# Optimization experiments

Hardware: AMD Instinct MI355X
Metric: run time of the kernel (lower is better)

## Reference

```python
import jax, jax.numpy as jnp
import numpy as np

IN_CH = 256
NUM_CLASSES = 1
CONF_THR = 0.3
NMS_IOU = 0.2
ANCHOR_SIZES = (32.0, 64.0, 128.0)
ASPECTS = (0.5, 1.0, 2.0)
NUM_ANCHORS = len(ANCHOR_SIZES) * len(ASPECTS)  # 9
K_CAND = 1024   # top-score candidates fed to NMS per image
MAX_DET = 100   # max_output_size in source
BN_EPS = 1e-5


def _anchors():
    a = [[s * r / 224.0, s / r / 224.0] for s in ANCHOR_SIZES for r in ASPECTS]
    return jnp.asarray(a, jnp.float32)  # [A, 2] (w, h)


def _conv(x, w, b, pad):
    y = jax.lax.conv_general_dilated(x, w, (1, 1), [(pad, pad), (pad, pad)],
                                     dimension_numbers=('NCHW', 'OIHW', 'NCHW'))
    return y + b[None, :, None, None]


def _bn(x, g, b, m, v):
    inv = jax.lax.rsqrt(v + BN_EPS)
    return (x - m[None, :, None, None]) * (g * inv)[None, :, None, None] + b[None, :, None, None]


def _corners(b):
    return (b[..., 0] - b[..., 2] / 2, b[..., 1] - b[..., 3] / 2,
            b[..., 0] + b[..., 2] / 2, b[..., 1] + b[..., 3] / 2)


def _iou_one(box, boxes):
    # box: [4] cxcywh, boxes: [K,4] -> iou [K]
    ax1, ay1, ax2, ay2 = _corners(box)
    bx1, by1, bx2, by2 = _corners(boxes)
    iw = jnp.maximum(jnp.minimum(ax2, bx2) - jnp.maximum(ax1, bx1), 0.0)
    ih = jnp.maximum(jnp.minimum(ay2, by2) - jnp.maximum(ay1, by1), 0.0)
    inter = iw * ih
    union = (ax2 - ax1) * (ay2 - ay1) + (bx2 - bx1) * (by2 - by1) - inter
    return inter / (union + 1e-16)


def _nms(boxes, scores):
    # boxes [K,4], scores [K] -> kept boxes padded to [MAX_DET,4]
    s0 = jnp.where(scores > CONF_THR, scores, -1.0)

    def body(i, carry):
        s, out = carry
        j = jnp.argmax(s)
        ok = s[j] > 0.0
        box = boxes[j]
        iou = _iou_one(box, boxes)
        s_new = jnp.where(iou > NMS_IOU, -1.0, s).at[j].set(-1.0)
        s = jnp.where(ok, s_new, s)
        out = out.at[i].set(jnp.where(ok, box, jnp.zeros_like(box)))
        return s, out

    _, out = jax.lax.fori_loop(0, MAX_DET, body,
                               (s0, jnp.zeros((MAX_DET, 4), boxes.dtype)))
    return out


def _forward(features, w1, b1, g1, be1, m1, v1, w2, b2, g2, be2, m2, v2, wo, bo):
    x = jax.nn.relu(_bn(_conv(features, w1, b1, 1), g1, be1, m1, v1))
    x = jax.nn.relu(_bn(_conv(x, w2, b2, 1), g2, be2, m2, v2))
    p = _conv(x, wo, bo, 0)                      # [B, A*(5+C), H, W]
    B, _, H, W = p.shape
    p = p.reshape(B, NUM_ANCHORS, 5 + NUM_CLASSES, H, W).transpose(0, 3, 4, 1, 2)  # [B,H,W,A,5+C]
    obj = jax.nn.sigmoid(p[..., 4])
    anch = _anchors()
    gx = jnp.arange(W, dtype=p.dtype)[None, :, None]
    gy = jnp.arange(H, dtype=p.dtype)[:, None, None]
    px = (jax.nn.sigmoid(p[..., 0]) + gx) / W
    py = (jax.nn.sigmoid(p[..., 1]) + gy) / H
    pw = jnp.exp(p[..., 2]) * anch[:, 0]
    ph = jnp.exp(p[..., 3]) * anch[:, 1]
    boxes = jnp.stack([px, py, pw, ph], -1).reshape(B, -1, 4)
    if NUM_CLASSES > 1:
        scores = obj * jax.nn.sigmoid(p[..., 5:]).max(-1)
    else:
        scores = obj
    scores = scores.reshape(B, -1)

    def per_image(bx, sc):
        top_s, idx = jax.lax.top_k(sc, K_CAND)
        return _nms(bx[idx], top_s)

    return jax.vmap(per_image)(boxes, scores)    # [B, MAX_DET, 4]


def setup_inputs() -> dict:
    key = jax.random.key(0)
    ks = jax.random.split(key, 16)
    B = 32
    c1, c2 = IN_CH // 2, IN_CH // 4
    oc = NUM_ANCHORS * (5 + NUM_CLASSES)
    return {
        'features': jax.random.normal(ks[0], (B, IN_CH, 56, 56), jnp.float32),
        'w1': jax.random.normal(ks[1], (c1, IN_CH, 3, 3), jnp.float32) * 0.02,
        'b1': jax.random.normal(ks[2], (c1,), jnp.float32) * 0.02,
        'g1': 1.0 + 0.1 * jax.random.normal(ks[3], (c1,), jnp.float32),
        'be1': 0.1 * jax.random.normal(ks[4], (c1,), jnp.float32),
        'm1': 0.1 * jax.random.normal(ks[5], (c1,), jnp.float32),
        'v1': jax.random.uniform(ks[6], (c1,), jnp.float32, 0.5, 1.5),
        'w2': jax.random.normal(ks[7], (c2, c1, 3, 3), jnp.float32) * 0.03,
        'b2': jax.random.normal(ks[8], (c2,), jnp.float32) * 0.02,
        'g2': 1.0 + 0.1 * jax.random.normal(ks[9], (c2,), jnp.float32),
        'be2': 0.1 * jax.random.normal(ks[10], (c2,), jnp.float32),
        'm2': 0.1 * jax.random.normal(ks[11], (c2,), jnp.float32),
        'v2': jax.random.uniform(ks[12], (c2,), jnp.float32, 0.5, 1.5),
        'wo': jax.random.normal(ks[13], (oc, c2, 1, 1), jnp.float32) * 0.1,
        'bo': jax.random.normal(ks[14], (oc,), jnp.float32) * 0.05,
    }


def reference(features, w1, b1, g1, be1, m1, v1, w2, b2, g2, be2, m2, v2, wo, bo):
    return _forward(features, w1, b1, g1, be1, m1, v1, w2, b2, g2, be2, m2, v2, wo, bo)
```

## Files before the change

### kernel.cpp

```cpp
#include <hip/hip_runtime.h>
#include <math.h>

constexpr int BB   = 32;
constexpr int HW   = 3136;
constexpr int C0   = 256, C1 = 128, C2 = 64;
constexpr int NA   = 9;
constexpr int NCAND = HW * NA;
constexpr int KSEL  = 1024;
constexpr int MAXDET = 100;

typedef _Float16 half8 __attribute__((ext_vector_type(8)));
typedef _Float16 half4v __attribute__((ext_vector_type(4)));
typedef float    f32x4  __attribute__((ext_vector_type(4)));
typedef float    f32x16 __attribute__((ext_vector_type(16)));

__global__ void bn_prep(const float* __restrict__ g, const float* __restrict__ be,
                        const float* __restrict__ m, const float* __restrict__ v,
                        const float* __restrict__ cb,
                        float* __restrict__ scl, float* __restrict__ tb, int n) {
    int i = threadIdx.x;
    if (i < n) {
        float inv = 1.f / sqrtf(v[i] + 1e-5f);
        float s = g[i] * inv;
        scl[i] = s;
        tb[i] = be[i] + (cb[i] - m[i]) * s;
    }
}

__global__ void reorder_w6(const float* __restrict__ w, _Float16* __restrict__ wc,
                           int CIN, int COUT) {
    int i = blockIdx.x * 256 + threadIdx.x;
    int K = CIN * 9;
    if (i >= 2 * COUT * K) return;
    int ci  = i & 31;
    int row = (i >> 5) % (2 * COUT);
    int ch  = (i >> 5) / (2 * COUT);
    int pl  = row / COUT;
    int oc  = row - pl * COUT;
    int cg = ch / 9, r = ch - cg * 9;
    int cin = cg * 32 + ci;
    float v = w[oc * K + cin * 9 + r];
    _Float16 h = (_Float16)v;
    wc[i] = pl ? (_Float16)(v - (float)h) : h;
}

__global__ __launch_bounds__(256) void nchw_to_nhwc_split(
    const float* __restrict__ in, _Float16* __restrict__ hi, _Float16* __restrict__ lo)
{
    __shared__ float tile[64 * 68];
    const int pt = blockIdx.x * 64, ct = blockIdx.y * 64, b = blockIdx.z;
    const int t = threadIdx.x;
    const int r0 = t >> 4, cidx = (t & 15) * 4;
#pragma unroll
    for (int rr = 0; rr < 64; rr += 16) {
        int r = rr + r0;
        const float* src = in + ((size_t)(b * 256 + ct + r)) * HW + pt + cidx;
        float4 v = *(const float4*)src;
        float* d = &tile[r * 68 + cidx];
        d[0] = v.x; d[1] = v.y; d[2] = v.z; d[3] = v.w;
    }
    __syncthreads();
    const int p = t >> 2, c0 = (t & 3) * 16;
    size_t obase = ((size_t)(b * HW + pt + p)) * 256 + ct + c0;
    half8 h0, h1, l0, l1;
#pragma unroll
    for (int j = 0; j < 16; ++j) {
        float v = tile[(c0 + j) * 68 + p];
        _Float16 hh = (_Float16)v;
        _Float16 ll = (_Float16)(v - (float)hh);
        if (j < 8) { h0[j] = hh; l0[j] = ll; }
        else       { h1[j - 8] = hh; l1[j - 8] = ll; }
    }
    *(half8*)(hi + obase)     = h0;
    *(half8*)(hi + obase + 8) = h1;
    *(half8*)(lo + obase)     = l0;
    *(half8*)(lo + obase + 8) = l1;
}

template <int CIN, int COUT, bool NHWC_OUT>
__global__ __launch_bounds__(256, 3) void conv3x3_v7(
    const _Float16* __restrict__ xhi,
    const _Float16* __restrict__ xlo,
    const _Float16* __restrict__ wc,
    const float* __restrict__ scl, const float* __restrict__ tb,
    _Float16* __restrict__ ohi,
    _Float16* __restrict__ olo,
    float* __restrict__ onchw)
{
    constexpr int K     = CIN * 9;
    constexpr int NCH   = K / 32;
    constexpr int WROWS = 2 * COUT;
    constexpr int WOC   = (COUT / 64) ? (COUT / 64) : 1;
    constexpr int PROW  = 72;
    constexpr int WROW  = 40;
    constexpr int WLDS  = WROWS / 64;

    __shared__ _Float16 SP[128 * PROW];
    __shared__ _Float16 SW[WROWS * WROW];

    const int bid = blockIdx.x;
    const int swz = (bid & 7) * (gridDim.x >> 3) + (bid >> 3);
    const int b = swz / 25;
    const int pixBase = (swz - b * 25) * 128;
    const int bHW = b * HW;

    const int t = threadIdx.x;

    const int p     = t & 127;
    const int plane = t >> 7;
    const int pixA  = pixBase + p;
    const int ya = pixA / 56, xa = pixA - ya * 56;
    const bool pv = pixA < HW;
    const _Float16* xsrc = plane ? xlo : xhi;

    const int l = t & 63;
    const int wid = t >> 6;
    const int wp = wid & 1, wo = wid >> 1;
    const int lc = l & 31, lk = l >> 5;

    f32x16 acc[2][WOC];
#pragma unroll
    for (int pi = 0; pi < 2; ++pi)
#pragma unroll
        for (int oi = 0; oi < WOC; ++oi) acc[pi][oi] = (f32x16)0.f;

    half8 pld[4];
    half8 wld[WLDS];

    auto stage_issue = [&](int ch) {
        int cg = ch / 9, r = ch - cg * 9;
        int ky = r / 3, kx = r - ky * 3;
        int iy = ya + ky - 1, ix = xa + kx - 1;
        bool valid = pv && ((unsigned)iy < 56u) && ((unsigned)ix < 56u);
        int sp = pixA + (ky - 1) * 56 + (kx - 1);
        const _Float16* src = xsrc + (valid ? ((size_t)(bHW + sp)) * CIN + cg * 32 : 0);
#pragma unroll
        for (int q = 0; q < 4; ++q) pld[q] = *(const half8*)(src + q * 8);
        if (!valid) {
#pragma unroll
            for (int q = 0; q < 4; ++q)
#pragma unroll
                for (int j = 0; j < 8; ++j) pld[q][j] = (_Float16)0.f;
        }
        const _Float16* wsA = wc + (size_t)ch * WROWS * 32 + t * (WLDS * 8);
#pragma unroll
        for (int q = 0; q < WLDS; ++q) wld[q] = *(const half8*)(wsA + q * 8);
    };
    auto stage_write = [&]() {
#pragma unroll
        for (int q = 0; q < 4; ++q)
            *(half8*)&SP[p * PROW + plane * 32 + q * 8] = pld[q];
#pragma unroll
        for (int q = 0; q < WLDS; ++q) {
            int h0 = t * (WLDS * 8) + q * 8;
            *(half8*)&SW[(h0 >> 5) * WROW + (h0 & 31)] = wld[q];
        }
    };

    stage_issue(0);
    stage_write();
    __syncthreads();

    for (int ch = 0; ch < NCH; ++ch) {
        const bool more = (ch + 1) < NCH;
        if (more) stage_issue(ch + 1);

#pragma unroll
        for (int ks = 0; ks < 2; ++ks) {
            half8 pb[2][2];
#pragma unroll
            for (int pi = 0; pi < 2; ++pi) {
                int prw = wp * 64 + pi * 32 + lc;
#pragma unroll
                for (int pl2 = 0; pl2 < 2; ++pl2)
                    pb[pi][pl2] = *(const half8*)&SP[prw * PROW + pl2 * 32 + ks * 16 + lk * 8];
            }
            half8 wa[WOC][2];
#pragma unroll
            for (int oi = 0; oi < WOC; ++oi) {
#pragma unroll
                for (int pl2 = 0; pl2 < 2; ++pl2) {
                    int row = pl2 * COUT + wo * (WOC * 32) + oi * 32 + lc;
                    wa[oi][pl2] = *(const half8*)&SW[row * WROW + ks * 16 + lk * 8];
                }
            }
#pragma unroll
            for (int pi = 0; pi < 2; ++pi)
#pragma unroll
                for (int oi = 0; oi < WOC; ++oi) {
                    acc[pi][oi] = __builtin_amdgcn_mfma_f32_32x32x16_f16(wa[oi][0], pb[pi][0], acc[pi][oi], 0, 0, 0);
                    acc[pi][oi] = __builtin_amdgcn_mfma_f32_32x32x16_f16(wa[oi][0], pb[pi][1], acc[pi][oi], 0, 0, 0);
                    acc[pi][oi] = __builtin_amdgcn_mfma_f32_32x32x16_f16(wa[oi][1], pb[pi][0], acc[pi][oi], 0, 0, 0);
                }
        }
        __syncthreads();
        if (more) {
            stage_write();
            __syncthreads();
        }
    }

#pragma unroll
    for (int pi = 0; pi < 2; ++pi) {
        const int pix = pixBase + wp * 64 + pi * 32 + lc;
        if (pix < HW) {
#pragma unroll
            for (int oi = 0; oi < WOC; ++oi) {
#pragma unroll
                for (int g = 0; g < 4; ++g) {
                    const int oc0 = wo * (WOC * 32) + oi * 32 + 8 * g + 4 * lk;
                    f32x4 s4 = *(const f32x4*)(scl + oc0);
                    f32x4 t4 = *(const f32x4*)(tb + oc0);
                    if constexpr (NHWC_OUT) {
                        half4v hh, ll;
#pragma unroll
                        for (int m2 = 0; m2 < 4; ++m2) {
                            float val = fmaxf(acc[pi][oi][g * 4 + m2] * s4[m2] + t4[m2], 0.f);
                            _Float16 h = (_Float16)val;
                            hh[m2] = h;
                            ll[m2] = (_Float16)(val - (float)h);
                        }
                        size_t o = ((size_t)(bHW + pix)) * COUT + oc0;
                        *(half4v*)(ohi + o) = hh;
                        *(half4v*)(olo + o) = ll;
                    } else {
#pragma unroll
                        for (int m2 = 0; m2 < 4; ++m2) {
                            float val = fmaxf(acc[pi][oi][g * 4 + m2] * s4[m2] + t4[m2], 0.f);
                            onchw[((size_t)(b * COUT + oc0 + m2)) * HW + pix] = val;
                        }
                    }
                }
            }
        }
    }
}

__global__ __launch_bounds__(256) void conv1x1_decode(
    const float* __restrict__ x2, const float* __restrict__ wo,
    const float* __restrict__ bo,
    float* __restrict__ boxes, float* __restrict__ scores)
{
    __shared__ float ws[64 * 56];
    for (int i = threadIdx.x; i < 54 * 64; i += 256) {
        int oc = i % 54, c = i / 54;
        ws[c * 56 + oc] = wo[oc * 64 + c];
    }
    __syncthreads();

    int u = blockIdx.x * 256 + threadIdx.x;
    int a = u % 9;
    int rest = u / 9;
    int quad = rest % 784;
    int b = rest / 784;
    int pix0 = quad * 4;
    int y = pix0 / 56;
    int x0 = pix0 - y * 56;

    const float* xb = x2 + (size_t)b * 64 * HW + pix0;
    float acc[5][4];
#pragma unroll
    for (int j = 0; j < 5; ++j)
#pragma unroll
        for (int p = 0; p < 4; ++p) acc[j][p] = 0.f;

#pragma unroll 8
    for (int c = 0; c < 64; ++c) {
        float4 xv = *(const float4*)(xb + c * HW);
#pragma unroll
        for (int j = 0; j < 5; ++j) {
            float w = ws[c * 56 + a * 6 + j];
            acc[j][0] += w * xv.x;
            acc[j][1] += w * xv.y;
            acc[j][2] += w * xv.z;
            acc[j][3] += w * xv.w;
        }
    }

    int si = a / 3, ri = a - si * 3;
    float sv = (float)(32 << si);
    float rv = 0.5f * (float)(1 << ri);
    float aw = (sv * rv) / 224.f;
    float ah = (sv / rv) / 224.f;
    float bo0 = bo[a * 6 + 0], bo1 = bo[a * 6 + 1], bo2 = bo[a * 6 + 2];
    float bo3 = bo[a * 6 + 3], bo4 = bo[a * 6 + 4];

#pragma unroll
    for (int p = 0; p < 4; ++p) {
        float p0 = acc[0][p] + bo0;
        float p1 = acc[1][p] + bo1;
        float p2 = acc[2][p] + bo2;
        float p3 = acc[3][p] + bo3;
        float p4 = acc[4][p] + bo4;
        float sx = 1.f / (1.f + expf(-p0));
        float sy = 1.f / (1.f + expf(-p1));
        float pxc = (sx + (float)(x0 + p)) / 56.f;
        float pyc = (sy + (float)y) / 56.f;
        float pw = expf(p2) * aw;
        float ph = expf(p3) * ah;
        float sc = 1.f / (1.f + expf(-p4));
        int n = (y * 56 + x0 + p) * 9 + a;
        float4 bx; bx.x = pxc; bx.y = pyc; bx.z = pw; bx.w = ph;
        *(float4*)&boxes[((size_t)b * NCAND + n) * 4] = bx;
        scores[(size_t)b * NCAND + n] = sc;
    }
}

__device__ __forceinline__ unsigned fkey(float f) {
    unsigned u = __float_as_uint(f);
    return (u & 0x80000000u) ? ~u : (u | 0x80000000u);
}

__global__ __launch_bounds__(1024) void topk_select(
    const float* __restrict__ scores, const float* __restrict__ boxes,
    float* __restrict__ cbox, float* __restrict__ csc, int* __restrict__ cidx)
{
    const int b = blockIdx.x, t = threadIdx.x;
    const float* sp = scores + (size_t)b * NCAND;
    const int lane = t & 63, w = t >> 6;

    __shared__ unsigned hist[256];
    __shared__ unsigned wsum[16];
    __shared__ unsigned s_sel, s_need, s_tot0, s_tot1;

    unsigned prefix = 0, maskSo = 0;
    int need = KSEL;

    for (int round = 0; round < 4; ++round) {
        int shift = 24 - round * 8;
        if (t < 256) hist[t] = 0;
        __syncthreads();
        for (int i = t; i < NCAND; i += 1024) {
            unsigned u = fkey(sp[i]);
            if ((u & maskSo) == prefix) atomicAdd(&hist[(u >> shift) & 255], 1u);
        }
        __syncthreads();
        if (t == 0) {
            int rem = need;
            unsigned sel = 0;
            for (int v = 255; v >= 0; --v) {
                int c = (int)hist[v];
                if (c >= rem) { sel = (unsigned)v; break; }
                rem -= c;
            }
            s_sel = sel; s_need = (unsigned)rem;
        }
        __syncthreads();
        prefix |= (s_sel << shift);
        maskSo |= (0xFFu << shift);
        need = (int)s_need;
        __syncthreads();
    }

    const unsigned cutoff = prefix;
    const unsigned needT = (unsigned)need;
    unsigned outBase = 0, tieBase = 0;
    const unsigned long long mlt = (1ull << lane) - 1ull;

    for (int c0 = 0; c0 < NCAND; c0 += 1024) {
        int i = c0 + t;
        bool valid = i < NCAND;
        float sc = valid ? sp[i] : 0.f;
        unsigned u = valid ? fkey(sc) : 0u;
        bool gt = valid && (u > cutoff);
        bool eq = valid && (u == cutoff);

        unsigned long long balE = __ballot(eq);
        unsigned lpE = (unsigned)__popcll(balE & mlt);
        if (lane == 0) wsum[w] = (unsigned)__popcll(balE);
        __syncthreads();
        if (t == 0) {
            unsigned run = 0;
            for (int k = 0; k < 16; ++k) { unsigned x = wsum[k]; wsum[k] = run; run += x; }
            s_tot1 = run;
        }
        __syncthreads();
        unsigned tieRank = tieBase + wsum[w] + lpE;
        bool take = gt || (eq && tieRank < needT);
        __syncthreads();

        unsigned long long balT = __ballot(take);
        unsigned lpT = (unsigned)__popcll(balT & mlt);
        if (lane == 0) wsum[w] = (unsigned)__popcll(balT);
        __syncthreads();
        if (t == 0) {
            unsigned run = 0;
            for (int k = 0; k < 16; ++k) { unsigned x = wsum[k]; wsum[k] = run; run += x; }
            s_tot0 = run;
        }
        __syncthreads();
        unsigned pos = outBase + wsum[w] + lpT;
        if (take) {
            float4 bx = *(const float4*)&boxes[((size_t)b * NCAND + i) * 4];
            *(float4*)&cbox[((size_t)b * KSEL + pos) * 4] = bx;
            csc[(size_t)b * KSEL + pos] = sc;
            cidx[(size_t)b * KSEL + pos] = i;
        }
        tieBase += s_tot1;
        outBase += s_tot0;
        __syncthreads();
    }
}

__global__ __launch_bounds__(64) void nms_wave(
    const float* __restrict__ cbox, const float* __restrict__ csc,
    const int* __restrict__ cidx, float* __restrict__ out)
{
    const int b = blockIdx.x, l = threadIdx.x;
    float cx[16], cy[16], w_[16], h_[16], s[16];
    int id[16];
#pragma unroll
    for (int j = 0; j < 16; ++j) {
        int ci = (b << 10) + (j << 6) + l;
        float4 bb = *(const float4*)&cbox[(size_t)ci * 4];
        float sc = csc[ci];
        cx[j] = bb.x; cy[j] = bb.y; w_[j] = bb.z; h_[j] = bb.w;
        s[j] = sc > 0.3f ? sc : -1.f;
        id[j] = cidx[ci];
    }
    float* ob = out + (size_t)b * MAXDET * 4;

    for (int it = 0; it < MAXDET; ++it) {
        float bs = s[0]; int bi = id[0];
        float bcx = cx[0], bcy = cy[0], bw = w_[0], bh = h_[0];
#pragma unroll
        for (int j = 1; j < 16; ++j) {
            bool tk = (s[j] > bs) || (s[j] == bs && id[j] < bi);
            if (tk) { bs = s[j]; bi = id[j]; bcx = cx[j]; bcy = cy[j]; bw = w_[j]; bh = h_[j]; }
        }
#pragma unroll
        for (int m2 = 1; m2 < 64; m2 <<= 1) {
            float os = __shfl_xor(bs, m2); int oi = __shfl_xor(bi, m2);
            float ox = __shfl_xor(bcx, m2), oy = __shfl_xor(bcy, m2);
            float ow = __shfl_xor(bw, m2), oh2 = __shfl_xor(bh, m2);
            bool tk = (os > bs) || (os == bs && oi < bi);
            if (tk) { bs = os; bi = oi; bcx = ox; bcy = oy; bw = ow; bh = oh2; }
        }
        if (bs <= 0.f) {
            for (int q = it * 4 + l; q < MAXDET * 4; q += 64) ob[q] = 0.f;
            break;
        }
        if (l == 0) {
            float4 o; o.x = bcx; o.y = bcy; o.z = bw; o.w = bh;
            *(float4*)&ob[it * 4] = o;
        }
        float wx1 = bcx - bw / 2.f, wy1 = bcy - bh / 2.f;
        float wx2 = bcx + bw / 2.f, wy2 = bcy + bh / 2.f;
        float war = (wx2 - wx1) * (wy2 - wy1);
#pragma unroll
        for (int j = 0; j < 16; ++j) {
            float jx1 = cx[j] - w_[j] / 2.f, jy1 = cy[j] - h_[j] / 2.f;
            float jx2 = cx[j] + w_[j] / 2.f, jy2 = cy[j] + h_[j] / 2.f;
            float iw = fminf(wx2, jx2) - fmaxf(wx1, jx1); iw = fmaxf(iw, 0.f);
            float ih = fminf(wy2, jy2) - fmaxf(wy1, jy1); ih = fmaxf(ih, 0.f);
            float inter = iw * ih;
            float jar = (jx2 - jx1) * (jy2 - jy1);
            float uni = war + jar - inter;
            if (inter / (uni + 1e-16f) > 0.2f) s[j] = -1.f;
        }
    }
}

extern "C" void kernel_launch(void* const* d_in, const int* in_sizes, int n_in,
                              void* d_out, int out_size, void* d_ws, size_t ws_size,
                              hipStream_t stream)
{
    const float* features = (const float*)d_in[0];
    const float* w1 = (const float*)d_in[1];
    const float* b1 = (const float*)d_in[2];
    const float* g1 = (const float*)d_in[3];
    const float* be1 = (const float*)d_in[4];
    const float* m1 = (const float*)d_in[5];
    const float* v1 = (const float*)d_in[6];
    const float* w2 = (const float*)d_in[7];
    const float* b2 = (const float*)d_in[8];
    const float* g2 = (const float*)d_in[9];
    const float* be2 = (const float*)d_in[10];
    const float* m2 = (const float*)d_in[11];
    const float* v2 = (const float*)d_in[12];
    const float* wo = (const float*)d_in[13];
    const float* bo = (const float*)d_in[14];

    char* ws = (char*)d_ws;
    size_t off = 0;
    auto alloc = [&](size_t bytes) {
        char* p = ws + off;
        off += (bytes + 255) / 256 * 256;
        return p;
    };

    _Float16* w1c = (_Float16*)alloc((size_t)2 * C1 * 2304 * 2);
    _Float16* w2c = (_Float16*)alloc((size_t)2 * C2 * 1152 * 2);
    float* scl1 = (float*)alloc(C1 * 4);
    float* tb1  = (float*)alloc(C1 * 4);
    float* scl2 = (float*)alloc(C2 * 4);
    float* tb2  = (float*)alloc(C2 * 4);

    const size_t planeF = (size_t)BB * HW * C0 * 2;
    char* regB = alloc(2 * planeF);
    _Float16* fhi = (_Float16*)regB;
    _Float16* flo = (_Float16*)(regB + planeF);

    const size_t planeX1 = (size_t)BB * HW * C1 * 2;
    char* regC = alloc(2 * planeX1);
    _Float16* x1hi = (_Float16*)regC;
    _Float16* x1lo = (_Float16*)(regC + planeX1);

    float* x2     = (float*)regB;
    float* boxes  = (float*)(regB + 25690112);
    float* scores = (float*)(regB + 25690112 + 14450688);
    float* cbox = (float*)regC;
    float* csc  = (float*)(regC + 524288);
    int*   cidx = (int*)(regC + 524288 + 131072);

    bn_prep<<<1, 256, 0, stream>>>(g1, be1, m1, v1, b1, scl1, tb1, C1);
    bn_prep<<<1, 256, 0, stream>>>(g2, be2, m2, v2, b2, scl2, tb2, C2);
    reorder_w6<<<(2 * C1 * 2304 + 255) / 256, 256, 0, stream>>>(w1, w1c, C0, C1);
    reorder_w6<<<(2 * C2 * 1152 + 255) / 256, 256, 0, stream>>>(w2, w2c, C1, C2);

    nchw_to_nhwc_split<<<dim3(49, 4, BB), 256, 0, stream>>>(features, fhi, flo);

    conv3x3_v7<C0, C1, true><<<800, 256, 0, stream>>>(
        fhi, flo, w1c, scl1, tb1, x1hi, x1lo, nullptr);
    conv3x3_v7<C1, C2, false><<<800, 256, 0, stream>>>(
        x1hi, x1lo, w2c, scl2, tb2, nullptr, nullptr, x2);

    conv1x1_decode<<<(BB * 784 * NA) / 256, 256, 0, stream>>>(x2, wo, bo, boxes, scores);

    topk_select<<<BB, 1024, 0, stream>>>(scores, boxes, cbox, csc, cidx);
    nms_wave<<<BB, 64, 0, stream>>>(cbox, csc, cidx, (float*)d_out);
}
```

Before: 705.8 us.

## Double-buffer conv3x3 LDS stages and parametrize wave tiling per layer

Converts the 3x3 conv kernel from single-buffered LDS with two barriers per K-chunk to a ping-pong double buffer with one barrier per chunk. Global loads are issued two chunks ahead, and MFMA compute runs at raised wave priority. The wave-to-pixel/output-channel split becomes a template parameter, so the second conv uses four pixel waves instead of two. Launch bounds drop from 3 to 2 blocks per CU, and the larger LDS footprint and register use may reduce occupancy.

```diff
diff --git a/kernel.cpp b/kernel.cpp
--- a/kernel.cpp
+++ b/kernel.cpp
@@ -77,8 +77,8 @@
     *(half8*)(lo + obase + 8) = l1;
 }
 
-template <int CIN, int COUT, bool NHWC_OUT>
-__global__ __launch_bounds__(256, 3) void conv3x3_v7(
+template <int CIN, int COUT, int WAVES_P, bool NHWC_OUT>
+__global__ __launch_bounds__(256, 2) void conv3x3_v9(
     const _Float16* __restrict__ xhi,
     const _Float16* __restrict__ xlo,
     const _Float16* __restrict__ wc,
@@ -89,14 +89,16 @@
 {
     constexpr int K     = CIN * 9;
     constexpr int NCH   = K / 32;
+    constexpr int WAVES_O = 4 / WAVES_P;
+    constexpr int PI    = 128 / (WAVES_P * 32);
+    constexpr int WOC   = COUT / (WAVES_O * 32);
     constexpr int WROWS = 2 * COUT;
-    constexpr int WOC   = (COUT / 64) ? (COUT / 64) : 1;
     constexpr int PROW  = 72;
     constexpr int WROW  = 40;
     constexpr int WLDS  = WROWS / 64;
 
-    __shared__ _Float16 SP[128 * PROW];
-    __shared__ _Float16 SW[WROWS * WROW];
+    __shared__ _Float16 SP[2][128 * PROW];
+    __shared__ _Float16 SW[2][WROWS * WROW];
 
     const int bid = blockIdx.x;
     const int swz = (bid & 7) * (gridDim.x >> 3) + (bid >> 3);
@@ -115,19 +117,16 @@
 
     const int l = t & 63;
     const int wid = t >> 6;
-    const int wp = wid & 1, wo = wid >> 1;
+    const int wp = wid % WAVES_P, wo = wid / WAVES_P;
     const int lc = l & 31, lk = l >> 5;
 
-    f32x16 acc[2][WOC];
-#pragma unroll
-    for (int pi = 0; pi < 2; ++pi)
+    f32x16 acc[PI][WOC];
+#pragma unroll
+    for (int pi = 0; pi < PI; ++pi)
 #pragma unroll
         for (int oi = 0; oi < WOC; ++oi) acc[pi][oi] = (f32x16)0.f;
 
-    half8 pld[4];
-    half8 wld[WLDS];
-
-    auto stage_issue = [&](int ch) {
+    auto issue = [&](int ch, half8 (&pld)[4], half8 (&wld)[WLDS]) {
         int cg = ch / 9, r = ch - cg * 9;
         int ky = r / 3, kx = r - ky * 3;
         int iy = ya + ky - 1, ix = xa + kx - 1;
@@ -146,46 +145,38 @@
 #pragma unroll
         for (int q = 0; q < WLDS; ++q) wld[q] = *(const half8*)(wsA + q * 8);
     };
-    auto stage_write = [&]() {
+    auto writeLDS = [&](int buf, half8 (&pld)[4], half8 (&wld)[WLDS]) {
 #pragma unroll
         for (int q = 0; q < 4; ++q)
-            *(half8*)&SP[p * PROW + plane * 32 + q * 8] = pld[q];
+            *(half8*)&SP[buf][p * PROW + plane * 32 + q * 8] = pld[q];
 #pragma unroll
         for (int q = 0; q < WLDS; ++q) {
             int h0 = t * (WLDS * 8) + q * 8;
-            *(half8*)&SW[(h0 >> 5) * WROW + (h0 & 31)] = wld[q];
+            *(half8*)&SW[buf][(h0 >> 5) * WROW + (h0 & 31)] = wld[q];
         }
     };
-
-    stage_issue(0);
-    stage_write();
-    __syncthreads();
-
-    for (int ch = 0; ch < NCH; ++ch) {
-        const bool more = (ch + 1) < NCH;
-        if (more) stage_issue(ch + 1);
-
+    auto compute = [&](int buf) {
+        __builtin_amdgcn_s_setprio(1);
 #pragma unroll
         for (int ks = 0; ks < 2; ++ks) {
-            half8 pb[2][2];
-#pragma unroll
-            for (int pi = 0; pi < 2; ++pi) {
-                int prw = wp * 64 + pi * 32 + lc;
+            half8 pb[PI][2];
+#pragma unroll
+            for (int pi = 0; pi < PI; ++pi) {
+                int prw = wp * (PI * 32) + pi * 32 + lc;
 #pragma unroll
                 for (int pl2 = 0; pl2 < 2; ++pl2)
-                    pb[pi][pl2] = *(const half8*)&SP[prw * PROW + pl2 * 32 + ks * 16 + lk * 8];
+                    pb[pi][pl2] = *(const half8*)&SP[buf][prw * PROW + pl2 * 32 + ks * 16 + lk * 8];
             }
             half8 wa[WOC][2];
 #pragma unroll
-            for (int oi = 0; oi < WOC; ++oi) {
+            for (int oi = 0; oi < WOC; ++oi)
 #pragma unroll
                 for (int pl2 = 0; pl2 < 2; ++pl2) {
                     int row = pl2 * COUT + wo * (WOC * 32) + oi * 32 + lc;
-                    wa[oi][pl2] = *(const half8*)&SW[row * WROW + ks * 16 + lk * 8];
+                    wa[oi][pl2] = *(const half8*)&SW[buf][row * WROW + ks * 16 + lk * 8];
                 }
-            }
-#pragma unroll
-            for (int pi = 0; pi < 2; ++pi)
+#pragma unroll
+            for (int pi = 0; pi < PI; ++pi)
 #pragma unroll
                 for (int oi = 0; oi < WOC; ++oi) {
                     acc[pi][oi] = __builtin_amdgcn_mfma_f32_32x32x16_f16(wa[oi][0], pb[pi][0], acc[pi][oi], 0, 0, 0);
@@ -193,16 +184,29 @@
                     acc[pi][oi] = __builtin_amdgcn_mfma_f32_32x32x16_f16(wa[oi][1], pb[pi][0], acc[pi][oi], 0, 0, 0);
                 }
         }
-        __syncthreads();
-        if (more) {
-            stage_write();
-            __syncthreads();
-        }
-    }
-
-#pragma unroll
-    for (int pi = 0; pi < 2; ++pi) {
-        const int pix = pixBase + wp * 64 + pi * 32 + lc;
+        __builtin_amdgcn_s_setprio(0);
+    };
+
+    half8 pA[4], wA[WLDS], pB[4], wB[WLDS];
+    issue(0, pA, wA);
+    writeLDS(0, pA, wA);
+    issue(1, pB, wB);
+    __syncthreads();
+
+    for (int ch = 0; ch < NCH; ch += 2) {
+        if (ch + 2 < NCH) issue(ch + 2, pA, wA);
+        compute(0);
+        writeLDS(1, pB, wB);
+        __syncthreads();
+        if (ch + 3 < NCH) issue(ch + 3, pB, wB);
+        compute(1);
+        if (ch + 2 < NCH) writeLDS(0, pA, wA);
+        __syncthreads();
+    }
+
+#pragma unroll
+    for (int pi = 0; pi < PI; ++pi) {
+        const int pix = pixBase + wp * (PI * 32) + pi * 32 + lc;
         if (pix < HW) {
 #pragma unroll
             for (int oi = 0; oi < WOC; ++oi) {
@@ -520,9 +524,9 @@
 
     nchw_to_nhwc_split<<<dim3(49, 4, BB), 256, 0, stream>>>(features, fhi, flo);
 
-    conv3x3_v7<C0, C1, true><<<800, 256, 0, stream>>>(
+    conv3x3_v9<C0, C1, 2, true><<<800, 256, 0, stream>>>(
         fhi, flo, w1c, scl1, tb1, x1hi, x1lo, nullptr);
-    conv3x3_v7<C1, C2, false><<<800, 256, 0, stream>>>(
+    conv3x3_v9<C1, C2, 4, false><<<800, 256, 0, stream>>>(
         x1hi, x1lo, w2c, scl2, tb2, nullptr, nullptr, x2);
 
     conv1x1_decode<<<(BB * 784 * NA) / 256, 256, 0, stream>>>(x2, wo, bo, boxes, scores);
```

Measured after the change: 691.0 us. 1.02x faster.
